# Kernel tuning notes

Hardware: AMD Instinct MI355X
Metric: run time of the kernel (lower is better)

## Reference

```python
import jax, jax.numpy as jnp
import numpy as np

EPS = 0.01       # l2-normalize epsilon
BN_EPS = 0.001   # batchnorm epsilon

def _l2norm(u):
    # tf.math.l2_normalize over axis=-2: x / sqrt(max(sum(x^2), eps))
    sq = jnp.sum(u * u, axis=-2, keepdims=True)
    return u / jnp.sqrt(jnp.maximum(sq, EPS))

def _dotprod(t, u):
    # einsum '...ij,...ik->...jk' contracting spatial axis, then flatten (C,C)->C*C
    d = jnp.einsum('bndi,bndj->bnij', t, _l2norm(u))
    return d.reshape(d.shape[0], d.shape[1], -1)

def _bn(x, gamma, beta):
    # inference-mode BN with moving_mean=0, moving_var=1 (fresh init)
    return gamma * (x / jnp.sqrt(1.0 + BN_EPS)) + beta

def setup_inputs() -> dict:
    key = jax.random.key(0)
    ks = jax.random.split(key, 9)
    B, N, D, C, BAS, U_IN, U_EQ = 8, 1024, 3, 64, 16, 512, 64
    F = 2 * C * C  # 8192 invariant features (2 input heads)
    t1 = jax.random.normal(ks[0], (B, N, D, C), dtype=jnp.float32)
    t2 = jax.random.normal(ks[1], (B, N, D, C), dtype=jnp.float32)
    u1 = jax.random.normal(ks[2], (B, N, D, C), dtype=jnp.float32)
    u2 = jax.random.normal(ks[3], (B, N, D, C), dtype=jnp.float32)
    V1 = jax.random.normal(ks[4], (B, N, D, BAS), dtype=jnp.float32)
    V2 = jax.random.normal(ks[5], (B, N, D, BAS), dtype=jnp.float32)
    W_inv = jax.random.normal(ks[6], (F, U_IN), dtype=jnp.float32) * 0.02
    b_inv = jnp.zeros((U_IN,), dtype=jnp.float32)
    g_inv = jnp.ones((U_IN,), dtype=jnp.float32)
    be_inv = jnp.zeros((U_IN,), dtype=jnp.float32)
    # two equivariant heads, each Dense(units=U_EQ*BAS)
    W_eq = jax.random.normal(ks[7], (2, F, U_EQ * BAS), dtype=jnp.float32) * 0.02
    b_eq = jnp.zeros((2, U_EQ * BAS), dtype=jnp.float32)
    g_eq = jnp.ones((2, U_EQ * BAS), dtype=jnp.float32)
    be_eq = jnp.zeros((2, U_EQ * BAS), dtype=jnp.float32)
    return {"t1": t1, "t2": t2, "u1": u1, "u2": u2, "V1": V1, "V2": V2,
            "W_inv": W_inv, "b_inv": b_inv, "g_inv": g_inv, "be_inv": be_inv,
            "W_eq": W_eq, "b_eq": b_eq, "g_eq": g_eq, "be_eq": be_eq}

def reference(t1, t2, u1, u2, V1, V2, W_inv, b_inv, g_inv, be_inv,
              W_eq, b_eq, g_eq, be_eq):
    # invariant features: concatenated flattened Gram blocks of the two heads
    feats = jnp.concatenate([_dotprod(t1, u1), _dotprod(t2, u2)], axis=-1)  # (B,N,F)
    # invariant branch: Dense -> BN -> ReLU
    invar = jax.nn.relu(_bn(feats @ W_inv + b_inv, g_inv, be_inv))  # (B,N,U_IN)
    # equivariant branch per head: Dense -> BN -> ReLU -> reshape -> basis recombine
    bas = V1.shape[-1]
    u_eq = W_eq.shape[-1] // bas
    eq_outs = []
    for l, V in enumerate((V1, V2)):
        wl = jax.nn.relu(_bn(feats @ W_eq[l] + b_eq[l], g_eq[l], be_eq[l]))
        wl = wl.reshape(wl.shape[0], wl.shape[1], u_eq, bas)  # (B,N,units,basis)
        # einsum '...ij,...mj->...mi': combine basis vectors -> (B,N,3,units)
        eq_outs.append(jnp.einsum('bnij,bnmj->bnmi', wl, V))
    eqvar = jnp.concatenate(eq_outs, axis=-1)  # (B,N,3,2*units)
    return invar, eqvar
```

## Files before the change

kernel.cpp:

```cpp
#include <hip/hip_runtime.h>
#include <hip/hip_bf16.h>

#define BROWS 8192
#define DDIM 3
#define CDIM 64
#define KF 8192
#define NINV 512
#define NEQ 1024
#define NTOT 2560
#define BAS 16
#define UEQ 64


typedef float f32x4 __attribute__((ext_vector_type(4)));
typedef __bf16 bf16x8_t __attribute__((ext_vector_type(8)));
typedef __bf16 bf16x4_t __attribute__((ext_vector_type(4)));

__device__ __forceinline__ void async_copy16(const void* g, void* l) {
    __builtin_amdgcn_global_load_lds(
        (__attribute__((address_space(1))) void*)(g),
        (__attribute__((address_space(3))) void*)(l), 16, 0, 0);
}

#define FROWS 16
#define FSTRIDE 196

__global__ __launch_bounds__(256) void feats_kernel(
    const float* __restrict__ t1, const float* __restrict__ t2,
    const float* __restrict__ u1, const float* __restrict__ u2,
    __hip_bfloat16* __restrict__ feats)
{
    __shared__ float sT1[FROWS * FSTRIDE];
    __shared__ float sT2[FROWS * FSTRIDE];
    __shared__ float sU1[FROWS * FSTRIDE];
    __shared__ float sU2[FROWS * FSTRIDE];

    const int tid = threadIdx.x;
    const int r0  = blockIdx.x * FROWS;

    #pragma unroll
    for (int k = 0; k < 12; ++k) {
        const int item = k * 256 + tid;
        const int r = item / 192, c = item - r * 192;
        const size_t g = (size_t)(r0 + r) * 192 + c;
        const int l = r * FSTRIDE + c;
        sT1[l] = t1[g];
        sT2[l] = t2[g];
        sU1[l] = u1[g];
        sU2[l] = u2[g];
    }
    __syncthreads();

    #pragma unroll
    for (int k = 0; k < 8; ++k) {
        const int item = k * 256 + tid;
        const int r = item >> 7, rem = item & 127;
        const int h = rem >> 6, c = rem & 63;
        float* U = (h ? sU2 : sU1) + r * FSTRIDE;
        float sq = U[c] * U[c] + U[64 + c] * U[64 + c] + U[128 + c] * U[128 + c];
        float s = 1.0f / sqrtf(fmaxf(sq, 0.01f));
        U[c] *= s; U[64 + c] *= s; U[128 + c] *= s;
    }
    __syncthreads();

    const int w       = tid >> 6;
    const int lane    = tid & 63;
    const int r_local = lane >> 2;
    const int p       = lane & 3;
    const int mb      = r0 >> 8;
    const int rloc0   = r0 & 255;
    const int rloc    = rloc0 + r_local;
    const int lc      = (p - (rloc >> 1)) & 3;
    const float* Tarr = (w >= 2 ? sT2 : sT1) + r_local * FSTRIDE;
    const float* Uarr = (w >= 2 ? sU2 : sU1) + r_local * FSTRIDE;

    char* dst = (char*)feats + (((size_t)(mb * 256 + w * 64)) << 14)
              + rloc0 * 64 + lane * 16;

    #pragma unroll 4
    for (int it = 0; it < 64; ++it) {
        const int kt = w * 64 + it;
        const int i  = (kt >> 1) & 63;
        const int jh = (kt & 1) * 32;
        const int j0 = jh + lc * 8;
        const float ti0 = Tarr[i], ti1 = Tarr[64 + i], ti2 = Tarr[128 + i];
        bf16x8_t vv;
        #pragma unroll
        for (int half = 0; half < 2; ++half) {
            const int j = j0 + half * 4;
            const float4 u0 = *reinterpret_cast<const float4*>(Uarr + j);
            const float4 u1_ = *reinterpret_cast<const float4*>(Uarr + 64 + j);
            const float4 u2_ = *reinterpret_cast<const float4*>(Uarr + 128 + j);
            vv[half * 4 + 0] = (__bf16)(ti0 * u0.x + ti1 * u1_.x + ti2 * u2_.x);
            vv[half * 4 + 1] = (__bf16)(ti0 * u0.y + ti1 * u1_.y + ti2 * u2_.y);
            vv[half * 4 + 2] = (__bf16)(ti0 * u0.z + ti1 * u1_.z + ti2 * u2_.z);
            vv[half * 4 + 3] = (__bf16)(ti0 * u0.w + ti1 * u1_.w + ti2 * u2_.w);
        }
        *reinterpret_cast<bf16x8_t*>(dst) = vv;
        dst += 16384;
    }
}

__global__ __launch_bounds__(256) void wt_kernel(
    const float* __restrict__ W_inv, const float* __restrict__ W_eq,
    __hip_bfloat16* __restrict__ WT)
{
    __shared__ float tile[32][33];
    const int tid = threadIdx.x;
    const int tx = tid & 31;
    const int ty = tid >> 5;
    const int n0 = blockIdx.x * 32;
    const int k0 = blockIdx.y * 32;

    const float* src; int ldn, nl0;
    if (n0 < NINV)            { src = W_inv;                       ldn = NINV; nl0 = n0; }
    else if (n0 < NINV + NEQ) { src = W_eq;                        ldn = NEQ;  nl0 = n0 - NINV; }
    else                      { src = W_eq + (size_t)KF * NEQ;     ldn = NEQ;  nl0 = n0 - NINV - NEQ; }

    #pragma unroll
    for (int i = 0; i < 4; ++i) {
        int kl = ty + i * 8;
        tile[kl][tx] = src[(size_t)(k0 + kl) * ldn + nl0 + tx];
    }
    __syncthreads();
    const int n_l = tid >> 3;
    const int k4  = (tid & 7) * 4;
    bf16x4_t v;
    #pragma unroll
    for (int q = 0; q < 4; ++q) v[q] = (__bf16)tile[k4 + q][n_l];

    const int n    = n0 + n_l;
    const int nb   = n / 320, rloc = n - nb * 320;
    const int kt   = k0 >> 5;
    const int lc   = (k4 >> 3) & 3, e = k4 & 7;
    const int phys = (lc + (rloc >> 1)) & 3;
    char* dst = (char*)WT + ((size_t)(nb * 256 + kt)) * 20480
              + rloc * 64 + phys * 16 + e * 2;
    *reinterpret_cast<bf16x4_t*>(dst) = v;
}

#define BM 256
#define BN 320
#define BK 32
#define ATILE 16384
#define BTILE 20480

__global__ __launch_bounds__(512, 2) void gemm_kernel(
    const __hip_bfloat16* __restrict__ A,
    const __hip_bfloat16* __restrict__ BT,
    const float* __restrict__ b_inv, const float* __restrict__ g_inv,
    const float* __restrict__ be_inv,
    const float* __restrict__ b_eq,  const float* __restrict__ g_eq,
    const float* __restrict__ be_eq,
    float* __restrict__ out_inv,
    float* __restrict__ Yeq)
{
    __shared__ alignas(16) __hip_bfloat16 AsBuf[4][BM * BK];
    __shared__ alignas(16) __hip_bfloat16 BsBuf[4][BN * BK];

    const int tid  = threadIdx.x;
    const int wave = tid >> 6;
    const int lane = tid & 63;
    const bool aWave = wave < 4;

    const int b    = blockIdx.x;
    const int xcd  = b & 7;
    const int slot = b >> 3;
    const int nb   = slot & 7;
    const int mb   = xcd * 4 + (slot >> 3);
    const int n0   = nb * BN;
    const int m0   = mb * BM;

    const char* pA = (const char*)A  + ((size_t)mb << 22);
    const char* pB = (const char*)BT + (size_t)nb * 256 * BTILE;

    const int aoff = wave * 4096 + lane * 16;
    const int boff = (wave - 4) * 5120 + lane * 16;

    const int chnk = (((lane >> 4) + ((lane & 15) >> 1)) & 3) * 8;
    const int wm = (wave & 3) * 64;
    const int wn = (wave >> 2) * 160;
    const int l15 = lane & 15;

    f32x4 acc[4][10] = {};

#define ISSUE(bufi, t)                                                        \
    do {                                                                      \
        if (aWave) {                                                          \
            _Pragma("unroll")                                                 \
            for (int j = 0; j < 4; ++j)                                       \
                async_copy16(pA + (size_t)(t) * ATILE + aoff + j * 1024,      \
                             (char*)&AsBuf[bufi][0] + aoff + j * 1024);       \
        } else {                                                              \
            _Pragma("unroll")                                                 \
            for (int j = 0; j < 5; ++j)                                       \
                async_copy16(pB + (size_t)(t) * BTILE + boff + j * 1024,      \
                             (char*)&BsBuf[bufi][0] + boff + j * 1024);       \
        }                                                                     \
    } while (0)

#define COMPUTE(bufi)                                                         \
    do {                                                                      \
        bf16x8_t a_[4];                                                       \
        _Pragma("unroll")                                                     \
        for (int mt = 0; mt < 4; ++mt)                                        \
            a_[mt] = *reinterpret_cast<const bf16x8_t*>(                      \
                &AsBuf[bufi][(wm + mt * 16 + l15) * BK + chnk]);              \
        _Pragma("unroll")                                                     \
        for (int nt = 0; nt < 10; ++nt) {                                     \
            bf16x8_t b_ = *reinterpret_cast<const bf16x8_t*>(                 \
                &BsBuf[bufi][(wn + nt * 16 + l15) * BK + chnk]);              \
            _Pragma("unroll")                                                 \
            for (int mt = 0; mt < 4; ++mt)                                    \
                acc[mt][nt] = __builtin_amdgcn_mfma_f32_16x16x32_bf16(        \
                    a_[mt], b_, acc[mt][nt], 0, 0, 0);                        \
        }                                                                     \
    } while (0)

#define WAITAB(na, nb_)                                                       \
    do {                                                                      \
        if (aWave) asm volatile("s_waitcnt vmcnt(" #na ")" ::: "memory");     \
        else       asm volatile("s_waitcnt vmcnt(" #nb_ ")" ::: "memory");    \
    } while (0)

#define MPHASE(b0, b1, t)                                                     \
    do {                                                                      \
        WAITAB(8, 10);                                                        \
        __builtin_amdgcn_s_barrier();                                         \
        asm volatile("" ::: "memory");                                        \
        COMPUTE(b0);                                                          \
        asm volatile("" ::: "memory");                                        \
        COMPUTE(b1);                                                          \
        asm volatile("" ::: "memory");                                        \
        __builtin_amdgcn_s_barrier();                                         \
        ISSUE(b0, t + 4);                                                     \
        ISSUE(b1, t + 5);                                                     \
    } while (0)

    ISSUE(0, 0);
    ISSUE(1, 1);
    ISSUE(2, 2);
    ISSUE(3, 3);

    for (int i = 0; i < 63; ++i) {
        const int t = i * 4;
        MPHASE(0, 1, t);
        MPHASE(2, 3, t + 2);
    }
    WAITAB(8, 10);
    __builtin_amdgcn_s_barrier();
    asm volatile("" ::: "memory");
    COMPUTE(0);
    asm volatile("" ::: "memory");
    COMPUTE(1);
    asm volatile("" ::: "memory");
    __builtin_amdgcn_s_barrier();

    asm volatile("s_waitcnt vmcnt(0)" ::: "memory");
    __builtin_amdgcn_s_barrier();
    asm volatile("" ::: "memory");
    COMPUTE(2);
    asm volatile("" ::: "memory");
    COMPUTE(3);

    const float RSQ = 0.9995003746877732f;
    #pragma unroll
    for (int nt = 0; nt < 10; ++nt) {
        const int gn = n0 + wn + nt * 16 + l15;
        float bbp, gg, bep;
        if (gn < NINV) {
            bbp = b_inv[gn]; gg = g_inv[gn]; bep = be_inv[gn];
        } else {
            const int e = gn - NINV, hh = e >> 10, nl = e & 1023;
            bbp = b_eq[hh * NEQ + nl]; gg = g_eq[hh * NEQ + nl]; bep = be_eq[hh * NEQ + nl];
        }
        gg *= RSQ;
        #pragma unroll
        for (int mt = 0; mt < 4; ++mt) {
            const int gmb = m0 + wm + mt * 16 + ((lane >> 4) << 2);
            #pragma unroll
            for (int rr = 0; rr < 4; ++rr) {
                float y = fmaxf(gg * (acc[mt][nt][rr] + bbp) + bep, 0.0f);
                const size_t gm = gmb + rr;
                if (gn < NINV) out_inv[gm * NINV + gn] = y;
                else           Yeq[gm * 2048 + (gn - NINV)] = y;
            }
        }
    }
#undef MPHASE
#undef WAITAB
#undef COMPUTE
#undef ISSUE
}

__global__ __launch_bounds__(128) void eqcomb_kernel(
    const float* __restrict__ Yeq,
    const float* __restrict__ V1, const float* __restrict__ V2,
    float* __restrict__ out_eq)
{
    const int row = blockIdx.x;
    const int tid = threadIdx.x;
    __shared__ float sV[2][DDIM][BAS];
    if (tid < 96) {
        const int h = tid / 48, rem = tid % 48;
        const float* V = h ? V2 : V1;
        sV[h][rem / BAS][rem % BAS] = V[(size_t)row * (DDIM * BAS) + rem];
    }
    __syncthreads();
    const int l = tid >> 6, u = tid & 63;
    const float4* y4 = reinterpret_cast<const float4*>(
        Yeq + (size_t)row * 2048 + l * 1024 + u * BAS);
    float a0 = 0.f, a1 = 0.f, a2 = 0.f;
    #pragma unroll
    for (int q = 0; q < 4; ++q) {
        float4 w = y4[q];
        const float* v0 = sV[l][0] + q * 4;
        const float* v1 = sV[l][1] + q * 4;
        const float* v2 = sV[l][2] + q * 4;
        a0 += w.x * v0[0] + w.y * v0[1] + w.z * v0[2] + w.w * v0[3];
        a1 += w.x * v1[0] + w.y * v1[1] + w.z * v1[2] + w.w * v1[3];
        a2 += w.x * v2[0] + w.y * v2[1] + w.z * v2[2] + w.w * v2[3];
    }
    float* o = out_eq + (size_t)row * (DDIM * 128);
    o[0 * 128 + l * 64 + u] = a0;
    o[1 * 128 + l * 64 + u] = a1;
    o[2 * 128 + l * 64 + u] = a2;
}

extern "C" void kernel_launch(void* const* d_in, const int* in_sizes, int n_in,
                              void* d_out, int out_size, void* d_ws, size_t ws_size,
                              hipStream_t stream) {
    const float* t1    = (const float*)d_in[0];
    const float* t2    = (const float*)d_in[1];
    const float* u1    = (const float*)d_in[2];
    const float* u2    = (const float*)d_in[3];
    const float* V1    = (const float*)d_in[4];
    const float* V2    = (const float*)d_in[5];
    const float* W_inv = (const float*)d_in[6];
    const float* b_inv = (const float*)d_in[7];
    const float* g_inv = (const float*)d_in[8];
    const float* be_inv= (const float*)d_in[9];
    const float* W_eq  = (const float*)d_in[10];
    const float* b_eq  = (const float*)d_in[11];
    const float* g_eq  = (const float*)d_in[12];
    const float* be_eq = (const float*)d_in[13];
    float* out = (float*)d_out;

    char* ws = (char*)d_ws;
    __hip_bfloat16* feats = (__hip_bfloat16*)(ws);
    __hip_bfloat16* WT    = (__hip_bfloat16*)(ws + 134217728);
    float*          Yeq   = (float*)(ws + 176160768);

    float* out_inv = out;
    float* out_eq  = out + (size_t)BROWS * NINV;

    hipLaunchKernelGGL(feats_kernel, dim3(BROWS / FROWS), dim3(256), 0, stream,
                       t1, t2, u1, u2, feats);
    hipLaunchKernelGGL(wt_kernel, dim3(NTOT / 32, KF / 32), dim3(256), 0, stream,
                       W_inv, W_eq, WT);
    hipLaunchKernelGGL(gemm_kernel, dim3((NTOT / BN) * (BROWS / BM)), dim3(512), 0, stream,
                       feats, WT, b_inv, g_inv, be_inv, b_eq, g_eq, be_eq,
                       out_inv, Yeq);
    hipLaunchKernelGGL(eqcomb_kernel, dim3(BROWS), dim3(128), 0, stream,
                       Yeq, V1, V2, out_eq);
}
```

Measured before the change: 546.4 us.

## Fuse basis recombination into GEMM epilogue, removing Yeq intermediate

Moves the equivariant basis recombination into the GEMM epilogue. Each block stages its rows of V1/V2 into reused shared memory and reduces the products across 16 lanes with shuffles. This removes the large fp32 Yeq intermediate write/read and the separate eqcomb launch, at the cost of extra epilogue shuffles, V loads per block, and scattered narrow stores.

```diff
diff --git a/kernel.cpp b/kernel.cpp
--- a/kernel.cpp
+++ b/kernel.cpp
@@ -152,11 +152,14 @@
     const float* __restrict__ be_inv,
     const float* __restrict__ b_eq,  const float* __restrict__ g_eq,
     const float* __restrict__ be_eq,
+    const float* __restrict__ V1,   const float* __restrict__ V2,
     float* __restrict__ out_inv,
-    float* __restrict__ Yeq)
+    float* __restrict__ out_eq)
 {
-    __shared__ alignas(16) __hip_bfloat16 AsBuf[4][BM * BK];
-    __shared__ alignas(16) __hip_bfloat16 BsBuf[4][BN * BK];
+    __shared__ alignas(16) char smem[147456];
+    auto* AsBuf = reinterpret_cast<__hip_bfloat16(*)[BM * BK]>(smem);
+    auto* BsBuf = reinterpret_cast<__hip_bfloat16(*)[BN * BK]>(smem + 65536);
+    float* sV   = reinterpret_cast<float*>(smem);
 
     const int tid  = threadIdx.x;
     const int wave = tid >> 6;
@@ -181,6 +184,7 @@
     const int wm = (wave & 3) * 64;
     const int wn = (wave >> 2) * 160;
     const int l15 = lane & 15;
+    const int q   = lane >> 4;
 
     f32x4 acc[4][10] = {};
 
@@ -263,27 +267,64 @@
     asm volatile("" ::: "memory");
     COMPUTE(3);
 
+    __syncthreads();
+    #pragma unroll
+    for (int k = 0; k < 48; ++k) {
+        const int e   = k * 512 + tid;
+        const int hh  = e / 12288;
+        const int rem = e - hh * 12288;
+        const int r   = rem / 48;
+        const int c   = rem - r * 48;
+        const int m   = c >> 4, j = c & 15;
+        const float v = (hh ? V2 : V1)[(size_t)(m0 + r) * 48 + c];
+        sV[((hh * 3 + m) * 256 + r) * 17 + j] = v;
+    }
+    __syncthreads();
+
     const float RSQ = 0.9995003746877732f;
     #pragma unroll
     for (int nt = 0; nt < 10; ++nt) {
         const int gn = n0 + wn + nt * 16 + l15;
-        float bbp, gg, bep;
         if (gn < NINV) {
-            bbp = b_inv[gn]; gg = g_inv[gn]; bep = be_inv[gn];
+            const float bbp = b_inv[gn];
+            const float gg  = g_inv[gn] * RSQ;
+            const float bep = be_inv[gn];
+            #pragma unroll
+            for (int mt = 0; mt < 4; ++mt) {
+                const int gmb = m0 + wm + mt * 16 + q * 4;
+                #pragma unroll
+                for (int rr = 0; rr < 4; ++rr) {
+                    float y = fmaxf(gg * (acc[mt][nt][rr] + bbp) + bep, 0.0f);
+                    out_inv[(size_t)(gmb + rr) * NINV + gn] = y;
+                }
+            }
         } else {
-            const int e = gn - NINV, hh = e >> 10, nl = e & 1023;
-            bbp = b_eq[hh * NEQ + nl]; gg = g_eq[hh * NEQ + nl]; bep = be_eq[hh * NEQ + nl];
-        }
-        gg *= RSQ;
-        #pragma unroll
-        for (int mt = 0; mt < 4; ++mt) {
-            const int gmb = m0 + wm + mt * 16 + ((lane >> 4) << 2);
+            const int e   = gn - NINV;
+            const int hh  = e >> 10;
+            const int el  = e & 1023;
+            const int uu  = el >> 4;
+            const float bbp = b_eq[hh * NEQ + el];
+            const float gg  = g_eq[hh * NEQ + el] * RSQ;
+            const float bep = be_eq[hh * NEQ + el];
             #pragma unroll
-            for (int rr = 0; rr < 4; ++rr) {
-                float y = fmaxf(gg * (acc[mt][nt][rr] + bbp) + bep, 0.0f);
-                const size_t gm = gmb + rr;
-                if (gn < NINV) out_inv[gm * NINV + gn] = y;
-                else           Yeq[gm * 2048 + (gn - NINV)] = y;
+            for (int mt = 0; mt < 4; ++mt) {
+                const int rl0 = wm + mt * 16 + q * 4;
+                #pragma unroll
+                for (int rr = 0; rr < 4; ++rr) {
+                    const float y = fmaxf(gg * (acc[mt][nt][rr] + bbp) + bep, 0.0f);
+                    const int rl = rl0 + rr;
+                    #pragma unroll
+                    for (int m = 0; m < 3; ++m) {
+                        float p = y * sV[((hh * 3 + m) * 256 + rl) * 17 + l15];
+                        p += __shfl_xor(p, 1);
+                        p += __shfl_xor(p, 2);
+                        p += __shfl_xor(p, 4);
+                        p += __shfl_xor(p, 8);
+                        if (l15 == 0)
+                            out_eq[(size_t)(m0 + rl) * 384 + m * 128
+                                   + hh * 64 + uu] = p;
+                    }
+                }
             }
         }
     }
@@ -291,40 +332,6 @@
 #undef WAITAB
 #undef COMPUTE
 #undef ISSUE
-}
-
-__global__ __launch_bounds__(128) void eqcomb_kernel(
-    const float* __restrict__ Yeq,
-    const float* __restrict__ V1, const float* __restrict__ V2,
-    float* __restrict__ out_eq)
-{
-    const int row = blockIdx.x;
-    const int tid = threadIdx.x;
-    __shared__ float sV[2][DDIM][BAS];
-    if (tid < 96) {
-        const int h = tid / 48, rem = tid % 48;
-        const float* V = h ? V2 : V1;
-        sV[h][rem / BAS][rem % BAS] = V[(size_t)row * (DDIM * BAS) + rem];
-    }
-    __syncthreads();
-    const int l = tid >> 6, u = tid & 63;
-    const float4* y4 = reinterpret_cast<const float4*>(
-        Yeq + (size_t)row * 2048 + l * 1024 + u * BAS);
-    float a0 = 0.f, a1 = 0.f, a2 = 0.f;
-    #pragma unroll
-    for (int q = 0; q < 4; ++q) {
-        float4 w = y4[q];
-        const float* v0 = sV[l][0] + q * 4;
-        const float* v1 = sV[l][1] + q * 4;
-        const float* v2 = sV[l][2] + q * 4;
-        a0 += w.x * v0[0] + w.y * v0[1] + w.z * v0[2] + w.w * v0[3];
-        a1 += w.x * v1[0] + w.y * v1[1] + w.z * v1[2] + w.w * v1[3];
-        a2 += w.x * v2[0] + w.y * v2[1] + w.z * v2[2] + w.w * v2[3];
-    }
-    float* o = out_eq + (size_t)row * (DDIM * 128);
-    o[0 * 128 + l * 64 + u] = a0;
-    o[1 * 128 + l * 64 + u] = a1;
-    o[2 * 128 + l * 64 + u] = a2;
 }
 
 extern "C" void kernel_launch(void* const* d_in, const int* in_sizes, int n_in,
@@ -349,7 +356,6 @@
     char* ws = (char*)d_ws;
     __hip_bfloat16* feats = (__hip_bfloat16*)(ws);
     __hip_bfloat16* WT    = (__hip_bfloat16*)(ws + 134217728);
-    float*          Yeq   = (float*)(ws + 176160768);
 
     float* out_inv = out;
     float* out_eq  = out + (size_t)BROWS * NINV;
@@ -360,7 +366,5 @@
                        W_inv, W_eq, WT);
     hipLaunchKernelGGL(gemm_kernel, dim3((NTOT / BN) * (BROWS / BM)), dim3(512), 0, stream,
                        feats, WT, b_inv, g_inv, be_inv, b_eq, g_eq, be_eq,
-                       out_inv, Yeq);
-    hipLaunchKernelGGL(eqcomb_kernel, dim3(BROWS), dim3(128), 0, stream,
-                       Yeq, V1, V2, out_eq);
-}
+                       V1, V2, out_inv, out_eq);
+}
```

Result: slower. 603.7 us (+10.5%).
